# Optimization experiments

Hardware: AMD Instinct MI355X
Metric: run time of the kernel (lower is better)

The kernel has to match this reference:

```python
import jax, jax.numpy as jnp
import numpy as np

N = 100_000      # nodes
E = 1_600_000    # edges (avg degree 16)
C_IN = 128
HID = 128        # 2 * out_channels
OUT = 64
EDIM = 1
NEG_SLOPE = 0.2  # PyG GATConv default negative_slope


def _gat(x, src, dst, n, W, a_s, a_d, b, edge_attr=None, We=None, a_e=None):
    """PyG GATConv with heads=1, concat=True, add_self_loops=True (fill_value='mean').
    x: [n, Cin]; src/dst: [E] (messages flow src -> dst); returns [n, Cout].
    """
    xl = x @ W                 # [n, Cout] transformed node features
    a_src = xl @ a_s           # [n] per-node source attention logit
    a_dst = xl @ a_d           # [n] per-node destination attention logit
    loop = jnp.arange(n)
    if edge_attr is not None:
        # self-loop edge_attr = mean of incoming edge_attr per node (fill_value='mean')
        ones = jnp.ones((src.shape[0],), xl.dtype)
        cnt = jax.ops.segment_sum(ones, dst, num_segments=n)              # [n]
        s = jax.ops.segment_sum(edge_attr, dst, num_segments=n)           # [n, EDIM]
        loop_attr = jnp.where(cnt[:, None] > 0, s / jnp.maximum(cnt, 1.0)[:, None], 0.0)
        ea = jnp.concatenate([edge_attr, loop_attr], axis=0)              # [E+n, EDIM]
    src2 = jnp.concatenate([src, loop])
    dst2 = jnp.concatenate([dst, loop])
    alpha = a_src[src2] + a_dst[dst2]                                      # [E+n]
    if edge_attr is not None:
        alpha = alpha + (ea @ We) @ a_e                                    # edge-attribute attention term
    alpha = jax.nn.leaky_relu(alpha, NEG_SLOPE)
    # softmax over incoming edges of each destination node (stable)
    m = jax.ops.segment_max(alpha, dst2, num_segments=n)
    ex = jnp.exp(alpha - m[dst2])
    den = jax.ops.segment_sum(ex, dst2, num_segments=n)
    coef = ex / den[dst2]                                                  # [E+n]
    out = jax.ops.segment_sum(coef[:, None] * xl[src2], dst2, num_segments=n)
    return out + b


def setup_inputs() -> dict:
    key = jax.random.key(0)
    ks = jax.random.split(key, 32)
    s = 0.1
    inp = {
        "x": jax.random.normal(ks[0], (N, C_IN), jnp.float32),
        "edge_index": jax.random.randint(ks[1], (2, E), 0, N, jnp.int64),
        "edge_weights": jax.random.uniform(ks[2], (E, EDIM), jnp.float32),
    }
    def lin(k, i, o):
        return jax.random.normal(k, (i, o), jnp.float32) * s
    def vec(k, c):
        return jax.random.normal(k, (c,), jnp.float32) * s
    # layer 0: 128 -> 128 (with edge attention)
    inp["W0"], inp["as0"], inp["ad0"] = lin(ks[3], C_IN, HID), vec(ks[4], HID), vec(ks[5], HID)
    inp["ae0"], inp["We0"], inp["b0"] = vec(ks[6], HID), lin(ks[7], EDIM, HID), jnp.zeros((HID,), jnp.float32)
    # layer 1: 128 -> 128 (with edge attention)
    inp["W1"], inp["as1"], inp["ad1"] = lin(ks[8], HID, HID), vec(ks[9], HID), vec(ks[10], HID)
    inp["ae1"], inp["We1"], inp["b1"] = vec(ks[11], HID), lin(ks[12], EDIM, HID), jnp.zeros((HID,), jnp.float32)
    # conv_mu: 128 -> 64 (with edge attention)
    inp["Wm"], inp["asm"], inp["adm"] = lin(ks[13], HID, OUT), vec(ks[14], OUT), vec(ks[15], OUT)
    inp["aem"], inp["Wem"], inp["bm"] = vec(ks[16], OUT), lin(ks[17], EDIM, OUT), jnp.zeros((OUT,), jnp.float32)
    # conv_logstd: 128 -> 64 (called WITHOUT edge_attr -> no edge term)
    inp["Wl"], inp["asl"], inp["adl"] = lin(ks[18], HID, OUT), vec(ks[19], OUT), vec(ks[20], OUT)
    inp["bl"] = jnp.zeros((OUT,), jnp.float32)
    return inp


def reference(x, edge_index, edge_weights,
              W0, as0, ad0, ae0, We0, b0,
              W1, as1, ad1, ae1, We1, b1,
              Wm, asm, adm, aem, Wem, bm,
              Wl, asl, adl, bl):
    src, dst = edge_index[0], edge_index[1]
    h = jax.nn.relu(_gat(x, src, dst, N, W0, as0, ad0, b0, edge_weights, We0, ae0))
    h = jax.nn.relu(_gat(h, src, dst, N, W1, as1, ad1, b1, edge_weights, We1, ae1))
    mu = _gat(h, src, dst, N, Wm, asm, adm, bm, edge_weights, Wem, aem)
    logstd = _gat(h, src, dst, N, Wl, asl, adl, bl)  # no edge_attr, per original forward
    return mu, logstd
```

## Files before the change

### kernel.cpp

```cpp
#include <hip/hip_runtime.h>

#define NN 100000
#define EE 1600000
#define NBK 782
#define NBKP 784
#define NBLK 391
#define NBLKP 392

typedef __attribute__((ext_vector_type(8))) __bf16 bf16x8;
typedef __attribute__((ext_vector_type(4))) float f32x4;
typedef unsigned short u16;

__device__ __forceinline__ float bf2f(u16 v) {
  union { unsigned u; float f; } x; x.u = ((unsigned)v) << 16; return x.f;
}
__device__ __forceinline__ u16 f2bf(float f) {
  union { unsigned u; float f; } x; x.f = f;
  x.u += 0x7fffu + ((x.u >> 16) & 1u);
  return (u16)(x.u >> 16);
}
__device__ __forceinline__ float lo_f(unsigned u) {
  union { unsigned u; float f; } x; x.u = u << 16; return x.f;
}
__device__ __forceinline__ float hi_f(unsigned u) {
  union { unsigned u; float f; } x; x.u = u & 0xffff0000u; return x.f;
}
__device__ __forceinline__ float lrelu(float x) { return x > 0.f ? x : 0.2f * x; }
__device__ __forceinline__ int clampi(int v, int hi) {
  return ((unsigned)v < (unsigned)hi) ? v : 0;
}
__device__ __forceinline__ float ldf(const void* p, size_t i, int fl) {
  return fl ? ((const float*)p)[i] : bf2f(((const u16*)p)[i]);
}

__device__ __forceinline__ int wave_fdetect(const u16* __restrict__ xb) {
  int lane = threadIdx.x & 63;
  int bad = 0;
#pragma unroll
  for (int j = 0; j < 4; ++j) {
    float a = fabsf(bf2f(xb[lane * 4 + j]));
    bad |= (!(a == a) || a > 1e6f) ? 1 : 0;
  }
  return (__ballot(bad) != 0ull) ? 1 : 0;
}
__device__ __forceinline__ int wave_mdetect(const int* __restrict__ ei) {
  int lane = threadIdx.x & 63;
  int v = (lane < 32) ? ei[2 * lane + 1] : 0;
  return (__ballot(v != 0) == 0ull) ? 1 : 0;
}

__global__ void k_fillf(float* __restrict__ o, int n, float v) {
  int i = blockIdx.x * 256 + threadIdx.x;
  if (i < n) o[i] = v;
}

struct CvtDesc { const void* src; u16* dst; int n; };
struct SetupArgs {
  CvtDesc cvt[12];
  const void* W[4]; u16* WT[4]; int WM[4];
  const void* dw[3]; const void* da[3]; int dm[3];
  float* cvals;
  const u16* xb;
};
__global__ __launch_bounds__(256) void k_setup(SetupArgs a) {
  int b = blockIdx.x, t = threadIdx.x;
  if (b < 12) {
    int fl = wave_fdetect(a.xb);
    const void* src = a.cvt[b].src; u16* dst = a.cvt[b].dst; int n = a.cvt[b].n;
    for (int i = t; i < n; i += 256)
      dst[i] = fl ? f2bf(((const float*)src)[i]) : ((const u16*)src)[i];
    return;
  }
  b -= 12;
  if (b < 192) {
    int fl = wave_fdetect(a.xb);
    int wsel, lb;
    if (b < 64)       { wsel = 0; lb = b; }
    else if (b < 128) { wsel = 1; lb = b - 64; }
    else if (b < 160) { wsel = 2; lb = b - 128; }
    else              { wsel = 3; lb = b - 160; }
    int M = a.WM[wsel];
    int i = lb * 256 + t;
    if (i < 128 * M) {
      int k = i / M, m = i % M;
      a.WT[wsel][m * 128 + k] = f2bf(ldf(a.W[wsel], i, fl));
    }
    return;
  }
  b -= 192;
  if (b < 3) {
    if (t < 64) {
      int fl = wave_fdetect(a.xb);
      float s = 0.f; int m = a.dm[b];
      for (int j = t; j < m; j += 64) s += ldf(a.dw[b], j, fl) * ldf(a.da[b], j, fl);
      for (int off = 32; off; off >>= 1) s += __shfl_xor(s, off);
      if (t == 0) a.cvals[b] = s;
    }
    return;
  }
}

__global__ __launch_bounds__(256) void k_ehist(const int* __restrict__ ei,
                                               int* __restrict__ histM) {
  __shared__ int h[NBKP];
  int blk = blockIdx.x, t = threadIdx.x;
  int m_ = wave_mdetect(ei);
  for (int j = t; j < NBKP; j += 256) h[j] = 0;
  __syncthreads();
#pragma unroll
  for (int j = 0; j < 16; ++j) {
    int e = blk * 4096 + j * 256 + t;
    if (e < EE) {
      int d = m_ ? ei[2 * (size_t)(EE + e)] : ei[EE + e];
      d = clampi(d, NN);
      atomicAdd(&h[d >> 7], 1);
    }
  }
  __syncthreads();
  for (int j = t; j < NBKP; j += 256) histM[j * NBLKP + blk] = h[j];
}

__global__ __launch_bounds__(512) void k_scanA(int* __restrict__ histM,
                                               int* __restrict__ binTot) {
  int b = blockIdx.x, t = threadIdx.x;
  int v = (t < NBLK) ? histM[b * NBLKP + t] : 0;
  int lane = t & 63, w = t >> 6;
  int sc = v;
  for (int off = 1; off < 64; off <<= 1) {
    int o = __shfl_up(sc, off); if (lane >= off) sc += o;
  }
  __shared__ int wt[8];
  if (lane == 63) wt[w] = sc;
  __syncthreads();
  int add = 0;
  for (int k = 0; k < w; ++k) add += wt[k];
  int excl = sc - v + add;
  if (t < NBLK) histM[b * NBLKP + t] = excl;
  if (t == 511) binTot[b] = excl;
}

__global__ __launch_bounds__(256) void k_scanB(const int* __restrict__ binTot,
                                               int* __restrict__ bucketBase,
                                               int* __restrict__ row_off) {
  int t = threadIdx.x;
  int v[4]; int s = 0;
#pragma unroll
  for (int j = 0; j < 4; ++j) {
    int idx = t * 4 + j;
    v[j] = (idx < NBK) ? binTot[idx] : 0;
    s += v[j];
  }
  int lane = t & 63, w = t >> 6;
  int sc = s;
  for (int off = 1; off < 64; off <<= 1) {
    int o = __shfl_up(sc, off); if (lane >= off) sc += o;
  }
  __shared__ int wt[4];
  if (lane == 63) wt[w] = sc;
  __syncthreads();
  int add = 0;
  for (int k = 0; k < w; ++k) add += wt[k];
  int ex = add + sc - s;
#pragma unroll
  for (int j = 0; j < 4; ++j) {
    int idx = t * 4 + j;
    if (idx <= NBK) bucketBase[idx] = ex;
    ex += v[j];
  }
  if (t == 0) row_off[NN] = EE;
}

__global__ __launch_bounds__(256) void k_escatter(
    const int* __restrict__ ei, const void* __restrict__ ew,
    const u16* __restrict__ xb, const int* __restrict__ histM,
    const int* __restrict__ bucketBase, int2* __restrict__ stage) {
  __shared__ int lbase[NBKP];
  __shared__ int cur[NBKP];
  int blk = blockIdx.x, t = threadIdx.x;
  int m_ = wave_mdetect(ei);
  int fl = wave_fdetect(xb);
  for (int j = t; j < NBKP; j += 256) {
    int bb = (j < NBK) ? (bucketBase[j] + histM[j * NBLKP + blk]) : 0;
    lbase[j] = bb; cur[j] = 0;
  }
  __syncthreads();
#pragma unroll
  for (int j = 0; j < 16; ++j) {
    int e = blk * 4096 + j * 256 + t;
    if (e < EE) {
      int s = m_ ? ei[2 * (size_t)e] : ei[e];
      int d = m_ ? ei[2 * (size_t)(EE + e)] : ei[EE + e];
      s = clampi(s, NN);
      d = clampi(d, NN);
      int bin = d >> 7, low = d & 127;
      int r = atomicAdd(&cur[bin], 1);
      int pos = lbase[bin] + r;
      if (pos >= 0 && pos < EE)
        stage[pos] = make_int2(s, (low << 16) | (int)f2bf(ldf(ew, e, fl)));
    }
  }
}

__global__ __launch_bounds__(256) void k_bucket(
    const int2* __restrict__ stage, const int* __restrict__ bucketBase,
    int2* __restrict__ edges, int* __restrict__ row_off, float* __restrict__ la) {
  __shared__ int hist[128];
  __shared__ float wsum[128];
  __shared__ int pref[128];
  __shared__ int cur[128];
  int b = blockIdx.x, t = threadIdx.x;
  int base = bucketBase[b], n = bucketBase[b + 1] - base;
  if (t < 128) { hist[t] = 0; wsum[t] = 0.f; cur[t] = 0; }
  __syncthreads();
  for (int i = t; i < n; i += 256) {
    int2 it = stage[base + i];
    int bin = (it.y >> 16) & 127;
    atomicAdd(&hist[bin], 1);
    atomicAdd(&wsum[bin], bf2f((u16)(it.y & 0xffff)));
  }
  __syncthreads();
  if (t == 0) {
    int run = 0;
    for (int j = 0; j < 128; ++j) { pref[j] = run; run += hist[j]; }
  }
  __syncthreads();
  if (t < 128) {
    int d = b * 128 + t;
    if (d < NN) {
      row_off[d] = base + pref[t];
      la[d] = hist[t] ? wsum[t] / (float)hist[t] : 0.f;
    }
  }
  for (int i = t; i < n; i += 256) {
    int2 it = stage[base + i];
    int bin = (it.y >> 16) & 127;
    int r = atomicAdd(&cur[bin], 1);
    edges[base + pref[bin] + r] = it;
  }
}

template<bool DUAL>
__device__ __forceinline__ void gemm_body(
    int bid, int fl, const void* __restrict__ Araw,
    const u16* __restrict__ WT,
    const u16* __restrict__ avs, const u16* __restrict__ avd,
    u16* __restrict__ xl,
    float* __restrict__ asrc, float* __restrict__ adst,
    float2* __restrict__ asAB, float* __restrict__ adstB, int n) {
  const int K = 128;
  int lane = threadIdx.x & 63;
  int wave = threadIdx.x >> 6;
  int quad = lane >> 4;
  int l16 = lane & 15;
  int r0 = (bid * 4 + wave) * 16;
  if (r0 >= n) return;
  int arow = r0 + l16; if (arow >= n) arow = n - 1;
  bf16x8 afr[4];
  if (fl) {
    const float* af = (const float*)Araw + (size_t)arow * K + quad * 8;
#pragma unroll
    for (int kb = 0; kb < 4; ++kb) {
      float4 f0 = *(const float4*)(af + kb * 32);
      float4 f1 = *(const float4*)(af + kb * 32 + 4);
      union { bf16x8 v; u16 s[8]; } t;
      t.s[0] = f2bf(f0.x); t.s[1] = f2bf(f0.y); t.s[2] = f2bf(f0.z); t.s[3] = f2bf(f0.w);
      t.s[4] = f2bf(f1.x); t.s[5] = f2bf(f1.y); t.s[6] = f2bf(f1.z); t.s[7] = f2bf(f1.w);
      afr[kb] = t.v;
    }
  } else {
    const u16* ab = (const u16*)Araw + (size_t)arow * K + quad * 8;
#pragma unroll
    for (int kb = 0; kb < 4; ++kb) afr[kb] = *(const bf16x8*)(ab + kb * 32);
  }
  f32x4 acc[8];
#pragma unroll
  for (int nb = 0; nb < 8; ++nb) acc[nb] = (f32x4){0.f, 0.f, 0.f, 0.f};
#pragma unroll
  for (int nb = 0; nb < 8; ++nb) {
    const u16* bbase = WT + (size_t)(nb * 16 + l16) * K + quad * 8;
#pragma unroll
    for (int kb = 0; kb < 4; ++kb) {
      bf16x8 bfr = *(const bf16x8*)(bbase + kb * 32);
      acc[nb] = __builtin_amdgcn_mfma_f32_16x16x32_bf16(afr[kb], bfr, acc[nb], 0, 0, 0);
    }
  }
  float ps[2][4] = {{0,0,0,0},{0,0,0,0}}, pd[2][4] = {{0,0,0,0},{0,0,0,0}};
#pragma unroll
  for (int nb = 0; nb < 8; ++nb) {
    const int g = (DUAL && nb >= 4) ? 1 : 0;
    int col = nb * 16 + l16;
    float vs = bf2f(avs[col]), vd = bf2f(avd[col]);
#pragma unroll
    for (int r = 0; r < 4; ++r) {
      int row = r0 + quad * 4 + r;
      float v = acc[nb][r];
      if (row < n) xl[(size_t)row * 128 + col] = f2bf(v);
      ps[g][r] += v * vs;
      pd[g][r] += v * vd;
    }
  }
#pragma unroll
  for (int off = 1; off < 16; off <<= 1) {
#pragma unroll
    for (int r = 0; r < 4; ++r) {
      ps[0][r] += __shfl_xor(ps[0][r], off);
      pd[0][r] += __shfl_xor(pd[0][r], off);
      if (DUAL) {
        ps[1][r] += __shfl_xor(ps[1][r], off);
        pd[1][r] += __shfl_xor(pd[1][r], off);
      }
    }
  }
  if (l16 == 0) {
#pragma unroll
    for (int r = 0; r < 4; ++r) {
      int row = r0 + quad * 4 + r;
      if (row < n) {
        if (DUAL) {
          asAB[row] = make_float2(ps[0][r], ps[1][r]);
          adst[row] = pd[0][r]; adstB[row] = pd[1][r];
        } else {
          asrc[row] = ps[0][r]; adst[row] = pd[0][r];
        }
      }
    }
  }
}

__global__ __launch_bounds__(256) void k_gemm0(
    const u16* __restrict__ xb, const void* __restrict__ Araw,
    const u16* __restrict__ WT, const u16* __restrict__ avs, const u16* __restrict__ avd,
    u16* __restrict__ xl, float* __restrict__ asrc, float* __restrict__ adst, int n) {
  int fl = wave_fdetect(xb);
  gemm_body<false>(blockIdx.x, fl, Araw, WT, avs, avd, xl, asrc, adst,
                   nullptr, nullptr, n);
}

template<bool DUAL>
__global__ __launch_bounds__(256) void k_gemm(
    const u16* __restrict__ A, const u16* __restrict__ WT,
    const u16* __restrict__ avs, const u16* __restrict__ avd,
    u16* __restrict__ xl, float* __restrict__ asrc, float* __restrict__ adst,
    float2* __restrict__ asAB, float* __restrict__ adstB, int n) {
  gemm_body<DUAL>(blockIdx.x, 0, A, WT, avs, avd, xl, asrc, adst, asAB, adstB, n);
}

__global__ __launch_bounds__(256) void k_agg(
    const int* __restrict__ row_off, const int2* __restrict__ edges,
    const float* __restrict__ asrc, const float* __restrict__ adst,
    const float* __restrict__ la, const float* __restrict__ cptr,
    const u16* __restrict__ xl, const u16* __restrict__ bias,
    u16* __restrict__ out, int n) {
  __shared__ float lp[4][64];
  __shared__ int lsv[4][64];
  int wid = (blockIdx.x * blockDim.x + threadIdx.x) >> 6;
  if (wid >= n) return;
  int w = threadIdx.x >> 6;
  int d = __builtin_amdgcn_readfirstlane(wid);
  int lane = threadIdx.x & 63;
  float c = cptr[0];
  float ad = adst[d];
  float aL = lrelu(asrc[d] + ad + c * la[d]);
  float lsum = 0.f;
  unsigned su = *(const unsigned*)(xl + (size_t)d * 128 + 2 * lane);
  float A0 = lo_f(su), A1 = hi_f(su);
  int beg = row_off[d], end = row_off[d + 1];
  for (int base = beg; base < end; base += 64) {
    int i = base + lane;
    bool v = i < end;
    int2 ev = v ? edges[i] : make_int2(0, 0);
    int s = ev.x;
    float e = 0.f;
    if (v) {
      float al = lrelu(asrc[s] + ad + c * bf2f((u16)(ev.y & 0xffff)));
      e = __expf(al - aL);
    }
    lsum += e;
    lp[w][lane] = e; lsv[w][lane] = s;
    int cnt = end - base; if (cnt > 64) cnt = 64;
    float B0 = 0.f, B1 = 0.f, C0 = 0.f, C1 = 0.f, D0 = 0.f, D1 = 0.f;
    int j = 0;
    for (; j + 4 <= cnt; j += 4) {
      float p0 = lp[w][j + 0]; int s0 = lsv[w][j + 0];
      float p1 = lp[w][j + 1]; int s1 = lsv[w][j + 1];
      float p2 = lp[w][j + 2]; int s2 = lsv[w][j + 2];
      float p3 = lp[w][j + 3]; int s3 = lsv[w][j + 3];
      unsigned u0 = *(const unsigned*)(xl + (size_t)s0 * 128 + 2 * lane);
      unsigned u1 = *(const unsigned*)(xl + (size_t)s1 * 128 + 2 * lane);
      unsigned u2 = *(const unsigned*)(xl + (size_t)s2 * 128 + 2 * lane);
      unsigned u3 = *(const unsigned*)(xl + (size_t)s3 * 128 + 2 * lane);
      A0 = fmaf(p0, lo_f(u0), A0); A1 = fmaf(p0, hi_f(u0), A1);
      B0 = fmaf(p1, lo_f(u1), B0); B1 = fmaf(p1, hi_f(u1), B1);
      C0 = fmaf(p2, lo_f(u2), C0); C1 = fmaf(p2, hi_f(u2), C1);
      D0 = fmaf(p3, lo_f(u3), D0); D1 = fmaf(p3, hi_f(u3), D1);
    }
    for (; j < cnt; ++j) {
      float p0 = lp[w][j]; int s0 = lsv[w][j];
      unsigned u0 = *(const unsigned*)(xl + (size_t)s0 * 128 + 2 * lane);
      A0 = fmaf(p0, lo_f(u0), A0); A1 = fmaf(p0, hi_f(u0), A1);
    }
    A0 += B0 + C0 + D0; A1 += B1 + C1 + D1;
  }
#pragma unroll
  for (int off = 32; off; off >>= 1) lsum += __shfl_xor(lsum, off);
  float inv = 1.f / (lsum + 1.f);
  float o0 = fmaxf(fmaf(A0, inv, bf2f(bias[2 * lane])), 0.f);
  float o1 = fmaxf(fmaf(A1, inv, bf2f(bias[2 * lane + 1])), 0.f);
  unsigned uo = (unsigned)f2bf(o0) | ((unsigned)f2bf(o1) << 16);
  *(unsigned*)(out + (size_t)d * 128 + 2 * lane) = uo;
}

__global__ __launch_bounds__(256) void k_aggh(
    const int* __restrict__ row_off, const int2* __restrict__ edges,
    const float2* __restrict__ asAB, const float* __restrict__ adA,
    const float* __restrict__ adB,
    const float* __restrict__ la, const float* __restrict__ cptr,
    const u16* __restrict__ xl, const u16* __restrict__ bias,
    float* __restrict__ outf, int n) {
  __shared__ float lpA[4][64];
  __shared__ float lpB[4][64];
  __shared__ int lsv[4][64];
  int wid = (blockIdx.x * blockDim.x + threadIdx.x) >> 6;
  if (wid >= n) return;
  int w = threadIdx.x >> 6;
  int d = __builtin_amdgcn_readfirstlane(wid);
  int lane = threadIdx.x & 63;
  bool isMu = lane < 32;
  float c = cptr[0];
  float adAd = adA[d], adBd = adB[d];
  float2 abd = asAB[d];
  float aLA = lrelu(abd.x + adAd + c * la[d]);
  float aLB = lrelu(abd.y + adBd);
  float lsA = 0.f, lsB = 0.f;
  unsigned su = *(const unsigned*)(xl + (size_t)d * 128 + 2 * lane);
  float A0 = lo_f(su), A1 = hi_f(su);
  int beg = row_off[d], end = row_off[d + 1];
  for (int base = beg; base < end; base += 64) {
    int i = base + lane;
    bool v = i < end;
    int2 ev = v ? edges[i] : make_int2(0, 0);
    int s = ev.x;
    float eA = 0.f, eB = 0.f;
    if (v) {
      float2 ab = asAB[s];
      eA = __expf(lrelu(ab.x + adAd + c * bf2f((u16)(ev.y & 0xffff))) - aLA);
      eB = __expf(lrelu(ab.y + adBd) - aLB);
    }
    lsA += eA; lsB += eB;
    lpA[w][lane] = eA; lpB[w][lane] = eB; lsv[w][lane] = s;
    const float* lpp = isMu ? lpA[w] : lpB[w];
    int cnt = end - base; if (cnt > 64) cnt = 64;
    float B0 = 0.f, B1 = 0.f, C0 = 0.f, C1 = 0.f, D0 = 0.f, D1 = 0.f;
    int j = 0;
    for (; j + 4 <= cnt; j += 4) {
      float p0 = lpp[j + 0]; int s0 = lsv[w][j + 0];
      float p1 = lpp[j + 1]; int s1 = lsv[w][j + 1];
      float p2 = lpp[j + 2]; int s2 = lsv[w][j + 2];
      float p3 = lpp[j + 3]; int s3 = lsv[w][j + 3];
      unsigned u0 = *(const unsigned*)(xl + (size_t)s0 * 128 + 2 * lane);
      unsigned u1 = *(const unsigned*)(xl + (size_t)s1 * 128 + 2 * lane);
      unsigned u2 = *(const unsigned*)(xl + (size_t)s2 * 128 + 2 * lane);
      unsigned u3 = *(const unsigned*)(xl + (size_t)s3 * 128 + 2 * lane);
      A0 = fmaf(p0, lo_f(u0), A0); A1 = fmaf(p0, hi_f(u0), A1);
      B0 = fmaf(p1, lo_f(u1), B0); B1 = fmaf(p1, hi_f(u1), B1);
      C0 = fmaf(p2, lo_f(u2), C0); C1 = fmaf(p2, hi_f(u2), C1);
      D0 = fmaf(p3, lo_f(u3), D0); D1 = fmaf(p3, hi_f(u3), D1);
    }
    for (; j < cnt; ++j) {
      float p0 = lpp[j]; int s0 = lsv[w][j];
      unsigned u0 = *(const unsigned*)(xl + (size_t)s0 * 128 + 2 * lane);
      A0 = fmaf(p0, lo_f(u0), A0); A1 = fmaf(p0, hi_f(u0), A1);
    }
    A0 += B0 + C0 + D0; A1 += B1 + C1 + D1;
  }
#pragma unroll
  for (int off = 32; off; off >>= 1) {
    lsA += __shfl_xor(lsA, off);
    lsB += __shfl_xor(lsB, off);
  }
  float inv = 1.f / ((isMu ? lsA : lsB) + 1.f);
  int col0 = 2 * lane;
  float o0 = fmaf(A0, inv, bf2f(bias[col0]));
  float o1 = fmaf(A1, inv, bf2f(bias[col0 + 1]));
  float* ob = isMu ? (outf + (size_t)d * 64 + col0)
                   : (outf + (size_t)NN * 64 + (size_t)d * 64 + (col0 - 64));
  ob[0] = o0; ob[1] = o1;
}

extern "C" void kernel_launch(void* const* d_in, const int* in_sizes, int n_in,
                              void* d_out, int out_size, void* d_ws, size_t ws_size,
                              hipStream_t stream) {
  (void)in_sizes; (void)n_in;
  const int* ei = (const int*)d_in[1];
  const u16* xb = (const u16*)d_in[0];
  float* outf = (float*)d_out;

  u16* regionA = (u16*)d_out;
  u16* regionB = (u16*)d_out + (size_t)NN * 128;
  int* histM = (int*)d_out;

  char* p = (char*)d_ws;
  auto alloc = [&](size_t bytes) -> char* {
    char* r = p; p += (bytes + 255) & ~(size_t)255; return r;
  };
  int*   row_off   = (int*)alloc((NN + 1) * 4);
  int*   binTot    = (int*)alloc(NBKP * 4);
  int*   bucketBase= (int*)alloc((NBKP + 2) * 4);
  float* la        = (float*)alloc(NN * 4);
  float* asrcA     = (float*)alloc(NN * 4);
  float* adstA     = (float*)alloc(NN * 4);
  float* adstB     = (float*)alloc(NN * 4);
  float2* asAB     = (float2*)alloc((size_t)NN * 8);
  int2*  edges     = (int2*)alloc((size_t)EE * 8);
  u16*   WT0       = (u16*)alloc(128 * 128 * 2);
  u16*   WT1       = (u16*)alloc(128 * 128 * 2);
  u16*   WTh       = (u16*)alloc(128 * 128 * 2);
  float* cvals     = (float*)alloc(16);
  u16*   vecc      = (u16*)alloc(9 * 256);
  u16*   xl        = (u16*)alloc((size_t)NN * 128 * 2);

  int2* stage = (int2*)xl;

  size_t NEED = (size_t)(p - (char*)d_ws);
  if (ws_size < NEED) {
    k_fillf<<<(out_size + 255) / 256, 256, 0, stream>>>(outf, out_size, 0.125f);
    return;
  }

  u16* as0c = vecc + 0 * 128; u16* ad0c = vecc + 1 * 128; u16* b0c = vecc + 2 * 128;
  u16* as1c = vecc + 3 * 128; u16* ad1c = vecc + 4 * 128; u16* b1c = vecc + 5 * 128;
  u16* hvs  = vecc + 6 * 128; u16* hvd  = vecc + 7 * 128; u16* bh  = vecc + 8 * 128;

  SetupArgs sa;
  sa.cvt[0]  = {d_in[4],  as0c, 128};
  sa.cvt[1]  = {d_in[5],  ad0c, 128};
  sa.cvt[2]  = {d_in[8],  b0c,  128};
  sa.cvt[3]  = {d_in[10], as1c, 128};
  sa.cvt[4]  = {d_in[11], ad1c, 128};
  sa.cvt[5]  = {d_in[14], b1c,  128};
  sa.cvt[6]  = {d_in[16], hvs,      64};
  sa.cvt[7]  = {d_in[22], hvs + 64, 64};
  sa.cvt[8]  = {d_in[17], hvd,      64};
  sa.cvt[9]  = {d_in[23], hvd + 64, 64};
  sa.cvt[10] = {d_in[20], bh,       64};
  sa.cvt[11] = {d_in[24], bh + 64,  64};
  sa.W[0] = d_in[3];  sa.WT[0] = WT0;            sa.WM[0] = 128;
  sa.W[1] = d_in[9];  sa.WT[1] = WT1;            sa.WM[1] = 128;
  sa.W[2] = d_in[15]; sa.WT[2] = WTh;            sa.WM[2] = 64;
  sa.W[3] = d_in[21]; sa.WT[3] = WTh + 64 * 128; sa.WM[3] = 64;
  sa.dw[0] = d_in[7];  sa.da[0] = d_in[6];  sa.dm[0] = 128;
  sa.dw[1] = d_in[13]; sa.da[1] = d_in[12]; sa.dm[1] = 128;
  sa.dw[2] = d_in[19]; sa.da[2] = d_in[18]; sa.dm[2] = 64;
  sa.cvals = cvals; sa.xb = xb;
  k_setup<<<12 + 192 + 3, 256, 0, stream>>>(sa);

  const int gblocks = (((NN + 15) / 16) + 3) / 4;
  const int eblocks = (int)(((size_t)NN * 64 + 255) / 256);

  k_ehist<<<NBLK, 256, 0, stream>>>(ei, histM);
  k_scanA<<<NBK, 512, 0, stream>>>(histM, binTot);
  k_scanB<<<1, 256, 0, stream>>>(binTot, bucketBase, row_off);
  k_escatter<<<NBLK, 256, 0, stream>>>(ei, d_in[2], xb, histM, bucketBase, stage);
  k_bucket<<<NBK, 256, 0, stream>>>(stage, bucketBase, edges, row_off, la);

  k_gemm0<<<gblocks, 256, 0, stream>>>(xb, d_in[0], WT0, as0c, ad0c,
                                       xl, asrcA, adstA, NN);
  k_agg<<<eblocks, 256, 0, stream>>>(row_off, edges, asrcA, adstA, la,
                                     cvals + 0, xl, b0c, regionB, NN);
  k_gemm<false><<<gblocks, 256, 0, stream>>>(regionB, WT1, as1c, ad1c,
                                             xl, asrcA, adstA, nullptr, nullptr, NN);
  k_agg<<<eblocks, 256, 0, stream>>>(row_off, edges, asrcA, adstA, la,
                                     cvals + 1, xl, b1c, regionA, NN);
  k_gemm<true><<<gblocks, 256, 0, stream>>>(regionA, WTh, hvs, hvd,
                                            xl, nullptr, adstA, asAB, adstB, NN);
  k_aggh<<<eblocks, 256, 0, stream>>>(row_off, edges, asAB, adstA, adstB,
                                      la, cvals + 2, xl, bh, outf, NN);
}
```

Measured before the change: 536.8 us.

## Aggregate each destination node with 16 lanes using 16-byte vector gathers

Measured after the change: 526.2 us. 1.02x faster.

```diff
diff --git a/kernel.cpp b/kernel.cpp
--- a/kernel.cpp
+++ b/kernel.cpp
@@ -24,6 +24,9 @@
 }
 __device__ __forceinline__ float hi_f(unsigned u) {
   union { unsigned u; float f; } x; x.u = u & 0xffff0000u; return x.f;
+}
+__device__ __forceinline__ unsigned pack2(float a, float b) {
+  return (unsigned)f2bf(a) | ((unsigned)f2bf(b) << 16);
 }
 __device__ __forceinline__ float lrelu(float x) { return x > 0.f ? x : 0.2f * x; }
 __device__ __forceinline__ int clampi(int v, int hi) {
@@ -351,63 +354,72 @@
     const float* __restrict__ la, const float* __restrict__ cptr,
     const u16* __restrict__ xl, const u16* __restrict__ bias,
     u16* __restrict__ out, int n) {
-  __shared__ float lp[4][64];
-  __shared__ int lsv[4][64];
-  int wid = (blockIdx.x * blockDim.x + threadIdx.x) >> 6;
-  if (wid >= n) return;
-  int w = threadIdx.x >> 6;
-  int d = __builtin_amdgcn_readfirstlane(wid);
-  int lane = threadIdx.x & 63;
+  __shared__ float lp[16][16];
+  __shared__ int lsv[16][16];
+  int tid = blockIdx.x * 256 + threadIdx.x;
+  int d = tid >> 4;
+  if (d >= n) return;
+  int l = threadIdx.x & 15;
+  int grp = threadIdx.x >> 4;
   float c = cptr[0];
   float ad = adst[d];
   float aL = lrelu(asrc[d] + ad + c * la[d]);
   float lsum = 0.f;
-  unsigned su = *(const unsigned*)(xl + (size_t)d * 128 + 2 * lane);
-  float A0 = lo_f(su), A1 = hi_f(su);
+  int4 su = *(const int4*)(xl + (size_t)d * 128 + l * 8);
+  float A0 = lo_f(su.x), A1 = hi_f(su.x), A2 = lo_f(su.y), A3 = hi_f(su.y);
+  float A4 = lo_f(su.z), A5 = hi_f(su.z), A6 = lo_f(su.w), A7 = hi_f(su.w);
+  float B0 = 0.f, B1 = 0.f, B2 = 0.f, B3 = 0.f, B4 = 0.f, B5 = 0.f, B6 = 0.f, B7 = 0.f;
   int beg = row_off[d], end = row_off[d + 1];
-  for (int base = beg; base < end; base += 64) {
-    int i = base + lane;
+  for (int base = beg; base < end; base += 16) {
+    int i = base + l;
     bool v = i < end;
     int2 ev = v ? edges[i] : make_int2(0, 0);
-    int s = ev.x;
     float e = 0.f;
-    if (v) {
-      float al = lrelu(asrc[s] + ad + c * bf2f((u16)(ev.y & 0xffff)));
-      e = __expf(al - aL);
-    }
+    if (v) e = __expf(lrelu(asrc[ev.x] + ad + c * bf2f((u16)(ev.y & 0xffff))) - aL);
     lsum += e;
-    lp[w][lane] = e; lsv[w][lane] = s;
-    int cnt = end - base; if (cnt > 64) cnt = 64;
-    float B0 = 0.f, B1 = 0.f, C0 = 0.f, C1 = 0.f, D0 = 0.f, D1 = 0.f;
+    lp[grp][l] = e; lsv[grp][l] = ev.x;
+    int cnt = end - base; if (cnt > 16) cnt = 16;
     int j = 0;
-    for (; j + 4 <= cnt; j += 4) {
-      float p0 = lp[w][j + 0]; int s0 = lsv[w][j + 0];
-      float p1 = lp[w][j + 1]; int s1 = lsv[w][j + 1];
-      float p2 = lp[w][j + 2]; int s2 = lsv[w][j + 2];
-      float p3 = lp[w][j + 3]; int s3 = lsv[w][j + 3];
-      unsigned u0 = *(const unsigned*)(xl + (size_t)s0 * 128 + 2 * lane);
-      unsigned u1 = *(const unsigned*)(xl + (size_t)s1 * 128 + 2 * lane);
-      unsigned u2 = *(const unsigned*)(xl + (size_t)s2 * 128 + 2 * lane);
-      unsigned u3 = *(const unsigned*)(xl + (size_t)s3 * 128 + 2 * lane);
-      A0 = fmaf(p0, lo_f(u0), A0); A1 = fmaf(p0, hi_f(u0), A1);
-      B0 = fmaf(p1, lo_f(u1), B0); B1 = fmaf(p1, hi_f(u1), B1);
-      C0 = fmaf(p2, lo_f(u2), C0); C1 = fmaf(p2, hi_f(u2), C1);
-      D0 = fmaf(p3, lo_f(u3), D0); D1 = fmaf(p3, hi_f(u3), D1);
-    }
-    for (; j < cnt; ++j) {
-      float p0 = lp[w][j]; int s0 = lsv[w][j];
-      unsigned u0 = *(const unsigned*)(xl + (size_t)s0 * 128 + 2 * lane);
-      A0 = fmaf(p0, lo_f(u0), A0); A1 = fmaf(p0, hi_f(u0), A1);
-    }
-    A0 += B0 + C0 + D0; A1 += B1 + C1 + D1;
-  }
-#pragma unroll
-  for (int off = 32; off; off >>= 1) lsum += __shfl_xor(lsum, off);
+    for (; j + 2 <= cnt; j += 2) {
+      float p0 = lp[grp][j];     int s0 = lsv[grp][j];
+      float p1 = lp[grp][j + 1]; int s1 = lsv[grp][j + 1];
+      int4 u0 = *(const int4*)(xl + (size_t)s0 * 128 + l * 8);
+      int4 u1 = *(const int4*)(xl + (size_t)s1 * 128 + l * 8);
+      A0 = fmaf(p0, lo_f(u0.x), A0); A1 = fmaf(p0, hi_f(u0.x), A1);
+      A2 = fmaf(p0, lo_f(u0.y), A2); A3 = fmaf(p0, hi_f(u0.y), A3);
+      A4 = fmaf(p0, lo_f(u0.z), A4); A5 = fmaf(p0, hi_f(u0.z), A5);
+      A6 = fmaf(p0, lo_f(u0.w), A6); A7 = fmaf(p0, hi_f(u0.w), A7);
+      B0 = fmaf(p1, lo_f(u1.x), B0); B1 = fmaf(p1, hi_f(u1.x), B1);
+      B2 = fmaf(p1, lo_f(u1.y), B2); B3 = fmaf(p1, hi_f(u1.y), B3);
+      B4 = fmaf(p1, lo_f(u1.z), B4); B5 = fmaf(p1, hi_f(u1.z), B5);
+      B6 = fmaf(p1, lo_f(u1.w), B6); B7 = fmaf(p1, hi_f(u1.w), B7);
+    }
+    if (j < cnt) {
+      float p0 = lp[grp][j]; int s0 = lsv[grp][j];
+      int4 u0 = *(const int4*)(xl + (size_t)s0 * 128 + l * 8);
+      A0 = fmaf(p0, lo_f(u0.x), A0); A1 = fmaf(p0, hi_f(u0.x), A1);
+      A2 = fmaf(p0, lo_f(u0.y), A2); A3 = fmaf(p0, hi_f(u0.y), A3);
+      A4 = fmaf(p0, lo_f(u0.z), A4); A5 = fmaf(p0, hi_f(u0.z), A5);
+      A6 = fmaf(p0, lo_f(u0.w), A6); A7 = fmaf(p0, hi_f(u0.w), A7);
+    }
+  }
+  A0 += B0; A1 += B1; A2 += B2; A3 += B3; A4 += B4; A5 += B5; A6 += B6; A7 += B7;
+#pragma unroll
+  for (int off = 1; off < 16; off <<= 1) lsum += __shfl_xor(lsum, off);
   float inv = 1.f / (lsum + 1.f);
-  float o0 = fmaxf(fmaf(A0, inv, bf2f(bias[2 * lane])), 0.f);
-  float o1 = fmaxf(fmaf(A1, inv, bf2f(bias[2 * lane + 1])), 0.f);
-  unsigned uo = (unsigned)f2bf(o0) | ((unsigned)f2bf(o1) << 16);
-  *(unsigned*)(out + (size_t)d * 128 + 2 * lane) = uo;
+  int4 bv = *(const int4*)(bias + l * 8);
+  float o0 = fmaxf(fmaf(A0, inv, lo_f((unsigned)bv.x)), 0.f);
+  float o1 = fmaxf(fmaf(A1, inv, hi_f((unsigned)bv.x)), 0.f);
+  float o2 = fmaxf(fmaf(A2, inv, lo_f((unsigned)bv.y)), 0.f);
+  float o3 = fmaxf(fmaf(A3, inv, hi_f((unsigned)bv.y)), 0.f);
+  float o4 = fmaxf(fmaf(A4, inv, lo_f((unsigned)bv.z)), 0.f);
+  float o5 = fmaxf(fmaf(A5, inv, hi_f((unsigned)bv.z)), 0.f);
+  float o6 = fmaxf(fmaf(A6, inv, lo_f((unsigned)bv.w)), 0.f);
+  float o7 = fmaxf(fmaf(A7, inv, hi_f((unsigned)bv.w)), 0.f);
+  int4 ov;
+  ov.x = (int)pack2(o0, o1); ov.y = (int)pack2(o2, o3);
+  ov.z = (int)pack2(o4, o5); ov.w = (int)pack2(o6, o7);
+  *(int4*)(out + (size_t)d * 128 + l * 8) = ov;
 }
 
 __global__ __launch_bounds__(256) void k_aggh(
@@ -417,74 +429,85 @@
     const float* __restrict__ la, const float* __restrict__ cptr,
     const u16* __restrict__ xl, const u16* __restrict__ bias,
     float* __restrict__ outf, int n) {
-  __shared__ float lpA[4][64];
-  __shared__ float lpB[4][64];
-  __shared__ int lsv[4][64];
-  int wid = (blockIdx.x * blockDim.x + threadIdx.x) >> 6;
-  if (wid >= n) return;
-  int w = threadIdx.x >> 6;
-  int d = __builtin_amdgcn_readfirstlane(wid);
-  int lane = threadIdx.x & 63;
-  bool isMu = lane < 32;
+  __shared__ float lpA[16][16];
+  __shared__ float lpB[16][16];
+  __shared__ int lsv[16][16];
+  int tid = blockIdx.x * 256 + threadIdx.x;
+  int d = tid >> 4;
+  if (d >= n) return;
+  int l = threadIdx.x & 15;
+  int grp = threadIdx.x >> 4;
+  bool isMu = l < 8;
   float c = cptr[0];
   float adAd = adA[d], adBd = adB[d];
   float2 abd = asAB[d];
   float aLA = lrelu(abd.x + adAd + c * la[d]);
   float aLB = lrelu(abd.y + adBd);
   float lsA = 0.f, lsB = 0.f;
-  unsigned su = *(const unsigned*)(xl + (size_t)d * 128 + 2 * lane);
-  float A0 = lo_f(su), A1 = hi_f(su);
+  int4 su = *(const int4*)(xl + (size_t)d * 128 + l * 8);
+  float A0 = lo_f(su.x), A1 = hi_f(su.x), A2 = lo_f(su.y), A3 = hi_f(su.y);
+  float A4 = lo_f(su.z), A5 = hi_f(su.z), A6 = lo_f(su.w), A7 = hi_f(su.w);
+  float B0 = 0.f, B1 = 0.f, B2 = 0.f, B3 = 0.f, B4 = 0.f, B5 = 0.f, B6 = 0.f, B7 = 0.f;
   int beg = row_off[d], end = row_off[d + 1];
-  for (int base = beg; base < end; base += 64) {
-    int i = base + lane;
+  for (int base = beg; base < end; base += 16) {
+    int i = base + l;
     bool v = i < end;
     int2 ev = v ? edges[i] : make_int2(0, 0);
-    int s = ev.x;
     float eA = 0.f, eB = 0.f;
     if (v) {
-      float2 ab = asAB[s];
+      float2 ab = asAB[ev.x];
       eA = __expf(lrelu(ab.x + adAd + c * bf2f((u16)(ev.y & 0xffff))) - aLA);
       eB = __expf(lrelu(ab.y + adBd) - aLB);
     }
     lsA += eA; lsB += eB;
-    lpA[w][lane] = eA; lpB[w][lane] = eB; lsv[w][lane] = s;
-    const float* lpp = isMu ? lpA[w] : lpB[w];
-    int cnt = end - base; if (cnt > 64) cnt = 64;
-    float B0 = 0.f, B1 = 0.f, C0 = 0.f, C1 = 0.f, D0 = 0.f, D1 = 0.f;
+    lpA[grp][l] = eA; lpB[grp][l] = eB; lsv[grp][l] = ev.x;
+    const float* lpp = isMu ? lpA[grp] : lpB[grp];
+    int cnt = end - base; if (cnt > 16) cnt = 16;
     int j = 0;
-    for (; j + 4 <= cnt; j += 4) {
-      float p0 = lpp[j + 0]; int s0 = lsv[w][j + 0];
-      float p1 = lpp[j + 1]; int s1 = lsv[w][j + 1];
-      float p2 = lpp[j + 2]; int s2 = lsv[w][j + 2];
-      float p3 = lpp[j + 3]; int s3 = lsv[w][j + 3];
-      unsigned u0 = *(const unsigned*)(xl + (size_t)s0 * 128 + 2 * lane);
-      unsigned u1 = *(const unsigned*)(xl + (size_t)s1 * 128 + 2 * lane);
-      unsigned u2 = *(const unsigned*)(xl + (size_t)s2 * 128 + 2 * lane);
-      unsigned u3 = *(const unsigned*)(xl + (size_t)s3 * 128 + 2 * lane);
-      A0 = fmaf(p0, lo_f(u0), A0); A1 = fmaf(p0, hi_f(u0), A1);
-      B0 = fmaf(p1, lo_f(u1), B0); B1 = fmaf(p1, hi_f(u1), B1);
-      C0 = fmaf(p2, lo_f(u2), C0); C1 = fmaf(p2, hi_f(u2), C1);
-      D0 = fmaf(p3, lo_f(u3), D0); D1 = fmaf(p3, hi_f(u3), D1);
-    }
-    for (; j < cnt; ++j) {
-      float p0 = lpp[j]; int s0 = lsv[w][j];
-      unsigned u0 = *(const unsigned*)(xl + (size_t)s0 * 128 + 2 * lane);
-      A0 = fmaf(p0, lo_f(u0), A0); A1 = fmaf(p0, hi_f(u0), A1);
-    }
-    A0 += B0 + C0 + D0; A1 += B1 + C1 + D1;
-  }
-#pragma unroll
-  for (int off = 32; off; off >>= 1) {
+    for (; j + 2 <= cnt; j += 2) {
+      float p0 = lpp[j];     int s0 = lsv[grp][j];
+      float p1 = lpp[j + 1]; int s1 = lsv[grp][j + 1];
+      int4 u0 = *(const int4*)(xl + (size_t)s0 * 128 + l * 8);
+      int4 u1 = *(const int4*)(xl + (size_t)s1 * 128 + l * 8);
+      A0 = fmaf(p0, lo_f(u0.x), A0); A1 = fmaf(p0, hi_f(u0.x), A1);
+      A2 = fmaf(p0, lo_f(u0.y), A2); A3 = fmaf(p0, hi_f(u0.y), A3);
+      A4 = fmaf(p0, lo_f(u0.z), A4); A5 = fmaf(p0, hi_f(u0.z), A5);
+      A6 = fmaf(p0, lo_f(u0.w), A6); A7 = fmaf(p0, hi_f(u0.w), A7);
+      B0 = fmaf(p1, lo_f(u1.x), B0); B1 = fmaf(p1, hi_f(u1.x), B1);
+      B2 = fmaf(p1, lo_f(u1.y), B2); B3 = fmaf(p1, hi_f(u1.y), B3);
+      B4 = fmaf(p1, lo_f(u1.z), B4); B5 = fmaf(p1, hi_f(u1.z), B5);
+      B6 = fmaf(p1, lo_f(u1.w), B6); B7 = fmaf(p1, hi_f(u1.w), B7);
+    }
+    if (j < cnt) {
+      float p0 = lpp[j]; int s0 = lsv[grp][j];
+      int4 u0 = *(const int4*)(xl + (size_t)s0 * 128 + l * 8);
+      A0 = fmaf(p0, lo_f(u0.x), A0); A1 = fmaf(p0, hi_f(u0.x), A1);
+      A2 = fmaf(p0, lo_f(u0.y), A2); A3 = fmaf(p0, hi_f(u0.y), A3);
+      A4 = fmaf(p0, lo_f(u0.z), A4); A5 = fmaf(p0, hi_f(u0.z), A5);
+      A6 = fmaf(p0, lo_f(u0.w), A6); A7 = fmaf(p0, hi_f(u0.w), A7);
+    }
+  }
+  A0 += B0; A1 += B1; A2 += B2; A3 += B3; A4 += B4; A5 += B5; A6 += B6; A7 += B7;
+#pragma unroll
+  for (int off = 1; off < 16; off <<= 1) {
     lsA += __shfl_xor(lsA, off);
     lsB += __shfl_xor(lsB, off);
   }
   float inv = 1.f / ((isMu ? lsA : lsB) + 1.f);
-  int col0 = 2 * lane;
-  float o0 = fmaf(A0, inv, bf2f(bias[col0]));
-  float o1 = fmaf(A1, inv, bf2f(bias[col0 + 1]));
-  float* ob = isMu ? (outf + (size_t)d * 64 + col0)
-                   : (outf + (size_t)NN * 64 + (size_t)d * 64 + (col0 - 64));
-  ob[0] = o0; ob[1] = o1;
+  int4 bv = *(const int4*)(bias + l * 8);
+  float4 oa, ob;
+  oa.x = fmaf(A0, inv, lo_f((unsigned)bv.x));
+  oa.y = fmaf(A1, inv, hi_f((unsigned)bv.x));
+  oa.z = fmaf(A2, inv, lo_f((unsigned)bv.y));
+  oa.w = fmaf(A3, inv, hi_f((unsigned)bv.y));
+  ob.x = fmaf(A4, inv, lo_f((unsigned)bv.z));
+  ob.y = fmaf(A5, inv, hi_f((unsigned)bv.z));
+  ob.z = fmaf(A6, inv, lo_f((unsigned)bv.w));
+  ob.w = fmaf(A7, inv, hi_f((unsigned)bv.w));
+  float* obase = isMu ? (outf + (size_t)d * 64 + l * 8)
+                      : (outf + (size_t)NN * 64 + (size_t)d * 64 + (l - 8) * 8);
+  *(float4*)obase = oa;
+  *(float4*)(obase + 4) = ob;
 }
 
 extern "C" void kernel_launch(void* const* d_in, const int* in_sizes, int n_in,
@@ -555,7 +578,7 @@
   k_setup<<<12 + 192 + 3, 256, 0, stream>>>(sa);
 
   const int gblocks = (((NN + 15) / 16) + 3) / 4;
-  const int eblocks = (int)(((size_t)NN * 64 + 255) / 256);
+  const int eblocks16 = (int)(((size_t)NN * 16 + 255) / 256);
 
   k_ehist<<<NBLK, 256, 0, stream>>>(ei, histM);
   k_scanA<<<NBK, 512, 0, stream>>>(histM, binTot);
@@ -565,14 +588,14 @@
 
   k_gemm0<<<gblocks, 256, 0, stream>>>(xb, d_in[0], WT0, as0c, ad0c,
                                        xl, asrcA, adstA, NN);
-  k_agg<<<eblocks, 256, 0, stream>>>(row_off, edges, asrcA, adstA, la,
-                                     cvals + 0, xl, b0c, regionB, NN);
+  k_agg<<<eblocks16, 256, 0, stream>>>(row_off, edges, asrcA, adstA, la,
+                                       cvals + 0, xl, b0c, regionB, NN);
   k_gemm<false><<<gblocks, 256, 0, stream>>>(regionB, WT1, as1c, ad1c,
                                              xl, asrcA, adstA, nullptr, nullptr, NN);
-  k_agg<<<eblocks, 256, 0, stream>>>(row_off, edges, asrcA, adstA, la,
-                                     cvals + 1, xl, b1c, regionA, NN);
+  k_agg<<<eblocks16, 256, 0, stream>>>(row_off, edges, asrcA, adstA, la,
+                                       cvals + 1, xl, b1c, regionA, NN);
   k_gemm<true><<<gblocks, 256, 0, stream>>>(regionA, WTh, hvs, hvd,
                                             xl, nullptr, adstA, asAB, adstB, NN);
-  k_aggh<<<eblocks, 256, 0, stream>>>(row_off, edges, asAB, adstA, adstB,
-                                      la, cvals + 2, xl, bh, outf, NN);
-}
+  k_aggh<<<eblocks16, 256, 0, stream>>>(row_off, edges, asAB, adstA, adstB,
+                                        la, cvals + 2, xl, bh, outf, NN);
+}
```
